# Optimization experiments

Hardware: AMD Instinct MI355X
Metric: run time of the kernel (lower is better)

The kernel has to match this reference:

```python
import jax, jax.numpy as jnp
import numpy as np

B, F, P, H, D = 2, 128, 256, 8, 64
DIM = H * D  # dim = num_heads * head_dim


def setup_inputs() -> dict:
    key = jax.random.key(0)
    ks = jax.random.split(key, 4)
    s = 0.02  # init scale for weights
    return {
        "x": jax.random.normal(ks[0], (B, F, P, DIM), jnp.float32),
        # frame QKV: projects dim -> (qkv, heads, dim_head)
        "W_f": (jax.random.normal(ks[1], (3, H, D, DIM), jnp.float32) * s),
        "b_f": jnp.zeros((3, H, D), jnp.float32),
        # point QKV: mixes (heads_in, dim_head_in) -> (qkv, heads_out, dim_head_out)
        "W_p": (jax.random.normal(ks[2], (3, H, D, H, D), jnp.float32) * s),
        "b_p": jnp.zeros((3, H, D), jnp.float32),
        # out projection: (heads, dim_head) -> dim
        "W_o": (jax.random.normal(ks[3], (H, D, DIM), jnp.float32) * s),
        "b_o": jnp.zeros((DIM,), jnp.float32),
    }


def reference(x, W_f, b_f, W_p, b_p, W_o, b_o):
    # ---- frame attention (attend across frames, per point) ----
    # qkv: [3, b, point, frame, heads, dim_head]
    qkv = jnp.einsum('bfpd,qhed->qbpfhe', x, W_f) + b_f[:, None, None, None, :, :]
    q, k, v = qkv[0], qkv[1], qkv[2]
    # scores: [b, point, frame_q, frame_k, heads]  (NOTE: source applies no 1/sqrt(d) scaling)
    scores = jnp.einsum('bpfhe,bpghe->bpfgh', q, k)
    w = jax.nn.softmax(scores, axis=3)  # softmax over frame_key
    fa = jnp.einsum('bpfgh,bpghe->bfphe', w, v)  # [b, frame, point, heads, dim_head]

    # ---- point attention (attend across points, per frame) ----
    # qkv2: [3, b, frame, point, heads, dim_head]
    qkv2 = jnp.einsum('bfpij,qheij->qbfphe', fa, W_p) + b_p[:, None, None, None, :, :]
    q2, k2, v2 = qkv2[0], qkv2[1], qkv2[2]
    # scores2: [b, frame, point_q, point_k, heads] (no scaling, per source)
    scores2 = jnp.einsum('bfphe,bfqhe->bfpqh', q2, k2)
    w2 = jax.nn.softmax(scores2, axis=3)  # softmax over point_key
    pa = jnp.einsum('bfpqh,bfqhe->bfphe', w2, v2)  # [b, frame, point, heads, dim_head]

    # ---- output projection ----
    return jnp.einsum('bfphe,hed->bfpd', pa, W_o) + b_o
```

## Files before the change

### kernel.cpp

```cpp
#include <hip/hip_runtime.h>
#include <hip/hip_bf16.h>
#include <stdint.h>

typedef __bf16 bf16;
typedef __attribute__((ext_vector_type(8))) __bf16 bf16x8;
typedef __attribute__((ext_vector_type(4))) __bf16 bf16x4;
typedef __attribute__((ext_vector_type(4))) float f32x4;

#define B_ 2
#define F_ 128
#define P_ 256
#define H_ 8
#define D_ 64
#define DIM_ 512
#define NROWS (B_*F_*P_)

__device__ __forceinline__ void load_lds16(const void* g, void* l) {
  __builtin_amdgcn_global_load_lds(
      (__attribute__((address_space(1))) void*)(uintptr_t)g,
      (__attribute__((address_space(3))) void*)(uint32_t)(uintptr_t)l,
      16, 0, 0);
}

__global__ void cvt_f32_bf16(const float* __restrict__ src, bf16* __restrict__ dst, int n)
{
  int i = (blockIdx.x * 256 + threadIdx.x) * 8;
  if (i < n) {
    float4 a = *(const float4*)(src + i);
    float4 b = *(const float4*)(src + i + 4);
    bf16x8 o;
    o[0] = (bf16)a.x; o[1] = (bf16)a.y; o[2] = (bf16)a.z; o[3] = (bf16)a.w;
    o[4] = (bf16)b.x; o[5] = (bf16)b.y; o[6] = (bf16)b.z; o[7] = (bf16)b.w;
    *(bf16x8*)(dst + i) = o;
  }
}

__global__ void transpose_wo(const float* __restrict__ src, bf16* __restrict__ dst)
{
  int idx = blockIdx.x * 256 + threadIdx.x;
  int d = idx & 511, he = idx >> 9;
  dst[(size_t)d * 512 + he] = (bf16)src[(size_t)he * 512 + d];
}

template <typename OutT, int NT>
__global__ __launch_bounds__(512, 2)
void gemm256(const bf16* __restrict__ A, const bf16* __restrict__ Bt,
             const float* __restrict__ bias, OutT* __restrict__ C)
{
  constexpr int K = 512;
  constexpr int N = NT * 256;
  constexpr int NTILES = 16;
  __shared__ __align__(16) bf16 As[4][256 * 32];
  __shared__ __align__(16) bf16 Bs[4][256 * 32];

  const int t    = threadIdx.x;
  const int lane = t & 63;
  const int l16  = lane & 15;
  const int qd   = lane >> 4;
  const int wave = t >> 6;
  const int wm   = wave >> 2;
  const int wn   = wave & 3;

  constexpr int NWG = NT * 256;
  const int logical = (blockIdx.x & 7) * (NWG / 8) + (blockIdx.x >> 3);
  const int mBase = (logical / NT) * 256;
  const int nBase = (logical % NT) * 256;

  const int srow = t >> 2;
  const int soct = (((t & 3) ^ ((srow >> 1) & 3)) << 3);
  const bf16* aS0 = A  + (size_t)(mBase + srow)       * K + soct;
  const bf16* aS1 = A  + (size_t)(mBase + srow + 128) * K + soct;
  const bf16* bS0 = Bt + (size_t)(nBase + srow)       * K + soct;
  const bf16* bS1 = Bt + (size_t)(nBase + srow + 128) * K + soct;
  const int dst = t * 8;

#define STAGE_A(tt) do { \
    load_lds16(aS0 + (tt) * 32, &As[(tt) & 3][dst]); \
    load_lds16(aS1 + (tt) * 32, &As[(tt) & 3][4096 + dst]); } while (0)
#define STAGE_B(tt) do { \
    load_lds16(bS0 + (tt) * 32, &Bs[(tt) & 3][dst]); \
    load_lds16(bS1 + (tt) * 32, &Bs[(tt) & 3][4096 + dst]); } while (0)

  const int swz = ((qd ^ ((l16 >> 1) & 3)) << 3);
  const bf16* aRd = &As[0][(wm * 128 + l16) * 32 + swz];
  const bf16* bRd = &Bs[0][(wn * 64  + l16) * 32 + swz];

  f32x4 acc[8][4] = {};

  STAGE_A(0); STAGE_B(0); STAGE_A(1); STAGE_B(1); STAGE_A(2); STAGE_B(2);

#define MF(i, j, av, bv) \
  acc[i][j] = __builtin_amdgcn_mfma_f32_16x16x32_bf16(av, bv, acc[i][j], 0, 0, 0)

#pragma unroll
  for (int tt = 0; tt < NTILES; ++tt) {
    if (tt + 3 < NTILES) STAGE_A(tt + 3);
    if      (tt <= NTILES - 4) asm volatile("s_waitcnt vmcnt(10)" ::: "memory");
    else if (tt == NTILES - 3) asm volatile("s_waitcnt vmcnt(8)"  ::: "memory");
    else if (tt == NTILES - 2) asm volatile("s_waitcnt vmcnt(4)"  ::: "memory");
    else                       asm volatile("s_waitcnt vmcnt(0)"  ::: "memory");
    __builtin_amdgcn_s_barrier();
    asm volatile("" ::: "memory");

    const bf16* aB = aRd + (tt & 3) * (256 * 32);
    const bf16* bB = bRd + (tt & 3) * (256 * 32);

    bf16x8 a[4], b[4];
#pragma unroll
    for (int j = 0; j < 4; ++j) b[j] = *(const bf16x8*)(bB + j * 512);
#pragma unroll
    for (int i = 0; i < 4; ++i) a[i] = *(const bf16x8*)(aB + i * 512);
    __builtin_amdgcn_s_setprio(1);
#pragma unroll
    for (int i = 0; i < 4; ++i)
#pragma unroll
      for (int j = 0; j < 4; ++j) MF(i, j, a[i], b[j]);
    __builtin_amdgcn_s_setprio(0);
    __builtin_amdgcn_s_barrier();
    asm volatile("" ::: "memory");

    if (tt + 3 < NTILES) STAGE_B(tt + 3);
#pragma unroll
    for (int i = 0; i < 4; ++i) a[i] = *(const bf16x8*)(aB + (4 + i) * 512);
    __builtin_amdgcn_s_setprio(1);
#pragma unroll
    for (int i = 0; i < 4; ++i)
#pragma unroll
      for (int j = 0; j < 4; ++j) MF(4 + i, j, a[i], b[j]);
    __builtin_amdgcn_s_setprio(0);
    __builtin_amdgcn_s_barrier();
    asm volatile("" ::: "memory");
  }
#undef STAGE_A
#undef STAGE_B
#undef MF

#pragma unroll
  for (int j = 0; j < 4; ++j) {
    const int coln = nBase + wn * 64 + j * 16 + l16;
    const float bv = bias[coln];
#pragma unroll
    for (int i = 0; i < 8; ++i) {
      const int rowm = mBase + wm * 128 + i * 16 + qd * 4;
#pragma unroll
      for (int r = 0; r < 4; ++r)
        C[(size_t)(rowm + r) * N + coln] = (OutT)(acc[i][j][r] + bv);
    }
  }
}

template <int NKT, int MODE, int VS>
__global__ __launch_bounds__(256, 2)
void attn2(const bf16* __restrict__ qkv, bf16* __restrict__ outp)
{
  __shared__ __align__(16) bf16 Vt[64 * VS];
  __shared__ __align__(16) bf16 Pq[128 * 136];

  const int t    = threadIdx.x;
  const int lane = t & 63;
  const int wave = t >> 6;
  const int l16  = lane & 15;
  const int qd   = lane >> 4;

  const int bid = blockIdx.x;
  int h, q0, rowbase, rstride;
  if (MODE == 0) {
    h = bid & 7;
    int p = (bid >> 3) & (P_ - 1);
    int b = bid >> 11;
    rowbase = b * F_ * P_ + p; rstride = P_; q0 = 0;
  } else {
    int qb = bid & 1;
    h = (bid >> 1) & 7;
    int f = (bid >> 4) & (F_ - 1);
    int b = bid >> 11;
    rowbase = (b * F_ + f) * P_; rstride = 1; q0 = qb * 128;
  }

#pragma unroll
  for (int p = 0; p < NKT / 8; ++p) {
    int key = p * 128 + (t >> 1);
    int eh  = (t & 1) * 32;
    const bf16* src = qkv + (size_t)(rowbase + key * rstride) * 1536 + 1024 + h * 64 + eh;
    bf16x8 v[4];
#pragma unroll
    for (int jj = 0; jj < 4; ++jj) v[jj] = *(const bf16x8*)(src + jj * 8);
#pragma unroll
    for (int jj = 0; jj < 4; ++jj)
#pragma unroll
      for (int j = 0; j < 8; ++j)
        Vt[(eh + jj * 8 + j) * VS + key] = v[jj][j];
  }

  const int qloc = wave * 32;
  bf16x8 qf[2][2];
#pragma unroll
  for (int qt = 0; qt < 2; ++qt)
#pragma unroll
    for (int ks = 0; ks < 2; ++ks)
      qf[qt][ks] = *(const bf16x8*)(qkv +
          (size_t)(rowbase + (q0 + qloc + qt * 16 + l16) * rstride) * 1536 +
          h * 64 + ks * 32 + qd * 8);

  f32x4 sacc[NKT][2] = {};
#pragma unroll
  for (int tn = 0; tn < NKT; ++tn) {
    const bf16* krow = qkv + (size_t)(rowbase + (tn * 16 + l16) * rstride) * 1536 + 512 + h * 64;
    bf16x8 kf0 = *(const bf16x8*)(krow + qd * 8);
    bf16x8 kf1 = *(const bf16x8*)(krow + 32 + qd * 8);
#pragma unroll
    for (int qt = 0; qt < 2; ++qt) {
      sacc[tn][qt] = __builtin_amdgcn_mfma_f32_16x16x32_bf16(kf0, qf[qt][0], sacc[tn][qt], 0, 0, 0);
      sacc[tn][qt] = __builtin_amdgcn_mfma_f32_16x16x32_bf16(kf1, qf[qt][1], sacc[tn][qt], 0, 0, 0);
    }
  }

#pragma unroll
  for (int qt = 0; qt < 2; ++qt) {
    float m = -3.0e38f;
#pragma unroll
    for (int tn = 0; tn < NKT; ++tn)
#pragma unroll
      for (int r = 0; r < 4; ++r) m = fmaxf(m, sacc[tn][qt][r]);
    m = fmaxf(m, __shfl_xor(m, 16));
    m = fmaxf(m, __shfl_xor(m, 32));
    float s = 0.0f;
#pragma unroll
    for (int tn = 0; tn < NKT; ++tn)
#pragma unroll
      for (int r = 0; r < 4; ++r) {
        float e0 = __expf(sacc[tn][qt][r] - m);
        sacc[tn][qt][r] = e0;
        s += e0;
      }
    s += __shfl_xor(s, 16);
    s += __shfl_xor(s, 32);
    float inv = 1.0f / s;
#pragma unroll
    for (int tn = 0; tn < NKT; ++tn)
#pragma unroll
      for (int r = 0; r < 4; ++r) sacc[tn][qt][r] *= inv;
  }

  f32x4 oacc[4][2] = {};
#pragma unroll
  for (int hf = 0; hf < NKT / 8; ++hf) {
#pragma unroll
    for (int qt = 0; qt < 2; ++qt)
#pragma unroll
      for (int tl = 0; tl < 8; ++tl) {
        int tn = hf * 8 + tl;
        bf16x4 pk;
#pragma unroll
        for (int r = 0; r < 4; ++r) pk[r] = (bf16)sacc[tn][qt][r];
        *(bf16x4*)(Pq + (qloc + qt * 16 + l16) * 136 + tl * 16 + qd * 4) = pk;
      }
    if (hf == 0) __syncthreads();
#pragma unroll
    for (int ks = 0; ks < 4; ++ks) {
      bf16x8 pf[2];
#pragma unroll
      for (int qt = 0; qt < 2; ++qt)
        pf[qt] = *(const bf16x8*)(Pq + (qloc + qt * 16 + l16) * 136 + ks * 32 + qd * 8);
#pragma unroll
      for (int te = 0; te < 4; ++te) {
        bf16x8 vf = *(const bf16x8*)(Vt + (te * 16 + l16) * VS + hf * 128 + ks * 32 + qd * 8);
#pragma unroll
        for (int qt = 0; qt < 2; ++qt)
          oacc[te][qt] = __builtin_amdgcn_mfma_f32_16x16x32_bf16(vf, pf[qt], oacc[te][qt], 0, 0, 0);
      }
    }
  }

#pragma unroll
  for (int te = 0; te < 4; ++te)
#pragma unroll
    for (int qt = 0; qt < 2; ++qt) {
      int q = q0 + qloc + qt * 16 + l16;
      bf16x4 pk;
#pragma unroll
      for (int r = 0; r < 4; ++r) pk[r] = (bf16)oacc[te][qt][r];
      *(bf16x4*)(outp + (size_t)(rowbase + q * rstride) * 512 + h * 64 + te * 16 + qd * 4) = pk;
    }
}

extern "C" void kernel_launch(void* const* d_in, const int* in_sizes, int n_in,
                              void* d_out, int out_size, void* d_ws, size_t ws_size,
                              hipStream_t stream)
{
  (void)in_sizes; (void)n_in; (void)out_size; (void)ws_size;
  const float* x   = (const float*)d_in[0];
  const float* Wf  = (const float*)d_in[1];
  const float* bfb = (const float*)d_in[2];
  const float* Wp  = (const float*)d_in[3];
  const float* bpb = (const float*)d_in[4];
  const float* Wo  = (const float*)d_in[5];
  const float* bob = (const float*)d_in[6];
  float* out = (float*)d_out;

  char* ws = (char*)d_ws;
  bf16* qkv = (bf16*)ws;
  bf16* fa  = (bf16*)(ws + (size_t)NROWS * 1536 * 2);
  bf16* xb  = fa;
  char* wbase = ws + (size_t)NROWS * 1536 * 2 + (size_t)NROWS * 512 * 2;
  bf16* wfb = (bf16*)wbase;
  bf16* wpb = (bf16*)(wbase + 1536 * 512 * 2);
  bf16* wot = (bf16*)(wbase + 2 * 1536 * 512 * 2);

  cvt_f32_bf16<<<(NROWS * 512) / (256 * 8), 256, 0, stream>>>(x, xb, NROWS * 512);
  cvt_f32_bf16<<<(1536 * 512) / (256 * 8), 256, 0, stream>>>(Wf, wfb, 1536 * 512);
  cvt_f32_bf16<<<(1536 * 512) / (256 * 8), 256, 0, stream>>>(Wp, wpb, 1536 * 512);
  transpose_wo<<<1024, 256, 0, stream>>>(Wo, wot);

  gemm256<bf16, 6><<<1536, 512, 0, stream>>>(xb, wfb, bfb, qkv);
  attn2<8, 0, 136><<<4096, 256, 0, stream>>>(qkv, fa);
  gemm256<bf16, 6><<<1536, 512, 0, stream>>>(fa, wpb, bpb, qkv);
  attn2<16, 1, 272><<<4096, 256, 0, stream>>>(qkv, fa);
  gemm256<float, 2><<<512, 512, 0, stream>>>(fa, wot, bob, out);
}
```

Measured before the change: 744.7 us.

## Double-buffer LDS fragment reads in GEMM to overlap with MFMA

Restructures the GEMM main loop so the LDS-to-register fragment loads for the next K tile are issued between the MFMA halves of the current tile, using double-buffered register fragments. Global-to-LDS staging of A and B is merged into one stage per iteration, and the waitcnt and barrier placement is adjusted to match. The aim is to hide LDS read latency behind MFMA work. In exchange it raises register pressure from the extra fragment buffers, which may lower occupancy under the existing launch bounds, and it depends on fragile barrier ordering to avoid overwriting LDS buffers that are still being read.

```diff
diff --git a/kernel.cpp b/kernel.cpp
--- a/kernel.cpp
+++ b/kernel.cpp
@@ -74,10 +74,9 @@
   const bf16* bS1 = Bt + (size_t)(nBase + srow + 128) * K + soct;
   const int dst = t * 8;
 
-#define STAGE_A(tt) do { \
+#define STAGE(tt) do { \
     load_lds16(aS0 + (tt) * 32, &As[(tt) & 3][dst]); \
-    load_lds16(aS1 + (tt) * 32, &As[(tt) & 3][4096 + dst]); } while (0)
-#define STAGE_B(tt) do { \
+    load_lds16(aS1 + (tt) * 32, &As[(tt) & 3][4096 + dst]); \
     load_lds16(bS0 + (tt) * 32, &Bs[(tt) & 3][dst]); \
     load_lds16(bS1 + (tt) * 32, &Bs[(tt) & 3][4096 + dst]); } while (0)
 
@@ -86,53 +85,72 @@
   const bf16* bRd = &Bs[0][(wn * 64  + l16) * 32 + swz];
 
   f32x4 acc[8][4] = {};
-
-  STAGE_A(0); STAGE_B(0); STAGE_A(1); STAGE_B(1); STAGE_A(2); STAGE_B(2);
+  bf16x8 la[2][4], lb[2][4], ha[2][4];
 
 #define MF(i, j, av, bv) \
   acc[i][j] = __builtin_amdgcn_mfma_f32_16x16x32_bf16(av, bv, acc[i][j], 0, 0, 0)
 
+  STAGE(0); STAGE(1); STAGE(2);
+  asm volatile("s_waitcnt vmcnt(8)" ::: "memory");
+  __builtin_amdgcn_s_barrier();
+  asm volatile("" ::: "memory");
+  __builtin_amdgcn_sched_barrier(0);
+#pragma unroll
+  for (int j = 0; j < 4; ++j) lb[0][j] = *(const bf16x8*)(bRd + j * 512);
+#pragma unroll
+  for (int i = 0; i < 4; ++i) la[0][i] = *(const bf16x8*)(aRd + i * 512);
+#pragma unroll
+  for (int i = 0; i < 4; ++i) ha[0][i] = *(const bf16x8*)(aRd + (4 + i) * 512);
+  __builtin_amdgcn_sched_barrier(0);
+
 #pragma unroll
   for (int tt = 0; tt < NTILES; ++tt) {
-    if (tt + 3 < NTILES) STAGE_A(tt + 3);
-    if      (tt <= NTILES - 4) asm volatile("s_waitcnt vmcnt(10)" ::: "memory");
-    else if (tt == NTILES - 3) asm volatile("s_waitcnt vmcnt(8)"  ::: "memory");
-    else if (tt == NTILES - 2) asm volatile("s_waitcnt vmcnt(4)"  ::: "memory");
-    else                       asm volatile("s_waitcnt vmcnt(0)"  ::: "memory");
-    __builtin_amdgcn_s_barrier();
-    asm volatile("" ::: "memory");
-
-    const bf16* aB = aRd + (tt & 3) * (256 * 32);
-    const bf16* bB = bRd + (tt & 3) * (256 * 32);
-
-    bf16x8 a[4], b[4];
-#pragma unroll
-    for (int j = 0; j < 4; ++j) b[j] = *(const bf16x8*)(bB + j * 512);
-#pragma unroll
-    for (int i = 0; i < 4; ++i) a[i] = *(const bf16x8*)(aB + i * 512);
+    const int cur = tt & 1, nxt = cur ^ 1;
+    const bf16* aN = aRd + ((tt + 1) & 3) * (256 * 32);
+    const bf16* bN = bRd + ((tt + 1) & 3) * (256 * 32);
+
+    if (tt + 3 < NTILES) STAGE(tt + 3);
+
     __builtin_amdgcn_s_setprio(1);
 #pragma unroll
     for (int i = 0; i < 4; ++i)
 #pragma unroll
-      for (int j = 0; j < 4; ++j) MF(i, j, a[i], b[j]);
+      for (int j = 0; j < 4; ++j) MF(i, j, la[cur][i], lb[cur][j]);
     __builtin_amdgcn_s_setprio(0);
-    __builtin_amdgcn_s_barrier();
-    asm volatile("" ::: "memory");
-
-    if (tt + 3 < NTILES) STAGE_B(tt + 3);
-#pragma unroll
-    for (int i = 0; i < 4; ++i) a[i] = *(const bf16x8*)(aB + (4 + i) * 512);
+
+    if (tt + 1 < NTILES) {
+      if      (tt <= NTILES - 4) asm volatile("s_waitcnt vmcnt(8)" ::: "memory");
+      else if (tt == NTILES - 3) asm volatile("s_waitcnt vmcnt(4)" ::: "memory");
+      else                       asm volatile("s_waitcnt vmcnt(0)" ::: "memory");
+      __builtin_amdgcn_s_barrier();
+      asm volatile("" ::: "memory");
+      __builtin_amdgcn_sched_barrier(0);
+#pragma unroll
+      for (int j = 0; j < 4; ++j) lb[nxt][j] = *(const bf16x8*)(bN + j * 512);
+      la[nxt][0] = *(const bf16x8*)(aN);
+      la[nxt][1] = *(const bf16x8*)(aN + 512);
+      __builtin_amdgcn_sched_barrier(0);
+    }
+
     __builtin_amdgcn_s_setprio(1);
 #pragma unroll
     for (int i = 0; i < 4; ++i)
 #pragma unroll
-      for (int j = 0; j < 4; ++j) MF(4 + i, j, a[i], b[j]);
+      for (int j = 0; j < 4; ++j) MF(4 + i, j, ha[cur][i], lb[cur][j]);
     __builtin_amdgcn_s_setprio(0);
-    __builtin_amdgcn_s_barrier();
-    asm volatile("" ::: "memory");
-  }
-#undef STAGE_A
-#undef STAGE_B
+
+    if (tt + 1 < NTILES) {
+      __builtin_amdgcn_s_barrier();
+      asm volatile("" ::: "memory");
+      __builtin_amdgcn_sched_barrier(0);
+      la[nxt][2] = *(const bf16x8*)(aN + 2 * 512);
+      la[nxt][3] = *(const bf16x8*)(aN + 3 * 512);
+#pragma unroll
+      for (int i = 0; i < 4; ++i) ha[nxt][i] = *(const bf16x8*)(aN + (4 + i) * 512);
+      __builtin_amdgcn_sched_barrier(0);
+    }
+  }
+#undef STAGE
 #undef MF
 
 #pragma unroll
```

Measured after the change: 741.8 us. Within noise of the previous version (-0.4%).

## Stage K in swizzled LDS via async loads and merge point-attention query blocks

Applied to the files above, without the earlier changes.

The attention kernel now loads K asynchronously into XOR-swizzled LDS with global_load_lds, so K is no longer read from global memory separately by each wave. The V global loads are issued before the QK MFMAs and their transposed LDS writes are deferred until after them, overlapping load latency with compute. Point attention now uses 512-thread blocks covering all 256 queries, so K/V are staged once per (frame, head) instead of twice. In exchange LDS use per block grows, which may lower occupancy, and correctness depends on the hand-placed vmcnt wait.

```diff
diff --git a/kernel.cpp b/kernel.cpp
--- a/kernel.cpp
+++ b/kernel.cpp
@@ -150,11 +150,15 @@
 }
 
 template <int NKT, int MODE, int VS>
-__global__ __launch_bounds__(256, 2)
-void attn2(const bf16* __restrict__ qkv, bf16* __restrict__ outp)
-{
+__global__ __launch_bounds__(MODE ? 512 : 256, 2)
+void attn3(const bf16* __restrict__ qkv, bf16* __restrict__ outp)
+{
+  constexpr int TB   = MODE ? 512 : 256;
+  constexpr int KEYS = NKT * 16;
+
+  __shared__ __align__(16) bf16 K_lds[KEYS * 64];
   __shared__ __align__(16) bf16 Vt[64 * VS];
-  __shared__ __align__(16) bf16 Pq[128 * 136];
+  __shared__ __align__(16) bf16 Pq[(TB / 2) * 136];
 
   const int t    = threadIdx.x;
   const int lane = t & 63;
@@ -163,34 +167,36 @@
   const int qd   = lane >> 4;
 
   const int bid = blockIdx.x;
-  int h, q0, rowbase, rstride;
+  int h, rowbase, rstride;
   if (MODE == 0) {
     h = bid & 7;
     int p = (bid >> 3) & (P_ - 1);
     int b = bid >> 11;
-    rowbase = b * F_ * P_ + p; rstride = P_; q0 = 0;
+    rowbase = b * F_ * P_ + p; rstride = P_;
   } else {
-    int qb = bid & 1;
-    h = (bid >> 1) & 7;
-    int f = (bid >> 4) & (F_ - 1);
-    int b = bid >> 11;
-    rowbase = (b * F_ + f) * P_; rstride = 1; q0 = qb * 128;
-  }
-
-#pragma unroll
-  for (int p = 0; p < NKT / 8; ++p) {
-    int key = p * 128 + (t >> 1);
-    int eh  = (t & 1) * 32;
-    const bf16* src = qkv + (size_t)(rowbase + key * rstride) * 1536 + 1024 + h * 64 + eh;
-    bf16x8 v[4];
-#pragma unroll
-    for (int jj = 0; jj < 4; ++jj) v[jj] = *(const bf16x8*)(src + jj * 8);
-#pragma unroll
-    for (int jj = 0; jj < 4; ++jj)
-#pragma unroll
-      for (int j = 0; j < 8; ++j)
-        Vt[(eh + jj * 8 + j) * VS + key] = v[jj][j];
-  }
+    h = bid & 7;
+    int f = (bid >> 3) & (F_ - 1);
+    int b = bid >> 10;
+    rowbase = (b * F_ + f) * P_; rstride = 1;
+  }
+
+  constexpr int KP = (KEYS * 8) / TB;
+#pragma unroll
+  for (int p = 0; p < KP; ++p) {
+    int gi  = p * TB + t;
+    int key = gi >> 3;
+    int oct = (gi & 7) ^ (key & 7);
+    load_lds16(qkv + (size_t)(rowbase + key * rstride) * 1536 + 512 + h * 64 + oct * 8,
+               K_lds + gi * 8);
+  }
+  __builtin_amdgcn_sched_barrier(0);
+
+  const int vkey = t >> 1;
+  const int eh   = (t & 1) * 32;
+  const bf16* vsrc = qkv + (size_t)(rowbase + vkey * rstride) * 1536 + 1024 + h * 64 + eh;
+  bf16x8 v[4];
+#pragma unroll
+  for (int jj = 0; jj < 4; ++jj) v[jj] = *(const bf16x8*)(vsrc + jj * 8);
 
   const int qloc = wave * 32;
   bf16x8 qf[2][2];
@@ -199,21 +205,34 @@
 #pragma unroll
     for (int ks = 0; ks < 2; ++ks)
       qf[qt][ks] = *(const bf16x8*)(qkv +
-          (size_t)(rowbase + (q0 + qloc + qt * 16 + l16) * rstride) * 1536 +
+          (size_t)(rowbase + (qloc + qt * 16 + l16) * rstride) * 1536 +
           h * 64 + ks * 32 + qd * 8);
+  __builtin_amdgcn_sched_barrier(0);
+
+  asm volatile("s_waitcnt vmcnt(8)" ::: "memory");
+  __builtin_amdgcn_s_barrier();
+  asm volatile("" ::: "memory");
 
   f32x4 sacc[NKT][2] = {};
 #pragma unroll
   for (int tn = 0; tn < NKT; ++tn) {
-    const bf16* krow = qkv + (size_t)(rowbase + (tn * 16 + l16) * rstride) * 1536 + 512 + h * 64;
-    bf16x8 kf0 = *(const bf16x8*)(krow + qd * 8);
-    bf16x8 kf1 = *(const bf16x8*)(krow + 32 + qd * 8);
+    int key = tn * 16 + l16;
+    const bf16* kr = K_lds + key * 64;
+    int s0 = ((qd ^ (key & 7)) << 3);
+    bf16x8 kf0 = *(const bf16x8*)(kr + s0);
+    bf16x8 kf1 = *(const bf16x8*)(kr + (s0 ^ 32));
 #pragma unroll
     for (int qt = 0; qt < 2; ++qt) {
       sacc[tn][qt] = __builtin_amdgcn_mfma_f32_16x16x32_bf16(kf0, qf[qt][0], sacc[tn][qt], 0, 0, 0);
       sacc[tn][qt] = __builtin_amdgcn_mfma_f32_16x16x32_bf16(kf1, qf[qt][1], sacc[tn][qt], 0, 0, 0);
     }
   }
+
+#pragma unroll
+  for (int jj = 0; jj < 4; ++jj)
+#pragma unroll
+    for (int j = 0; j < 8; ++j)
+      Vt[(eh + jj * 8 + j) * VS + vkey] = v[jj][j];
 
 #pragma unroll
   for (int qt = 0; qt < 2; ++qt) {
@@ -276,7 +295,7 @@
   for (int te = 0; te < 4; ++te)
 #pragma unroll
     for (int qt = 0; qt < 2; ++qt) {
-      int q = q0 + qloc + qt * 16 + l16;
+      int q = qloc + qt * 16 + l16;
       bf16x4 pk;
 #pragma unroll
       for (int r = 0; r < 4; ++r) pk[r] = (bf16)oacc[te][qt][r];
@@ -313,8 +332,8 @@
   transpose_wo<<<1024, 256, 0, stream>>>(Wo, wot);
 
   gemm256<bf16, 6><<<1536, 512, 0, stream>>>(xb, wfb, bfb, qkv);
-  attn2<8, 0, 136><<<4096, 256, 0, stream>>>(qkv, fa);
+  attn3<8, 0, 136><<<4096, 256, 0, stream>>>(qkv, fa);
   gemm256<bf16, 6><<<1536, 512, 0, stream>>>(fa, wpb, bpb, qkv);
-  attn2<16, 1, 272><<<4096, 256, 0, stream>>>(qkv, fa);
+  attn3<16, 1, 272><<<2048, 512, 0, stream>>>(qkv, fa);
   gemm256<float, 2><<<512, 512, 0, stream>>>(fa, wot, bob, out);
 }
```

New measurement: 705.1 us. 1.06x faster.
